# Performance work log

Hardware: AMD Instinct MI355X
Metric: run time of the kernel (lower is better)

## Reference

```python
import jax, jax.numpy as jnp
from jax import lax
import numpy as np

SIGMA = 5.0
ALPHA = 50.0
RADIUS = int(4.0 * SIGMA + 0.5)  # scipy gaussian_filter truncate=4.0 -> 20


def _gauss_kernel():
    t = jnp.arange(-RADIUS, RADIUS + 1, dtype=jnp.float32)
    phi = jnp.exp(-0.5 * (t / SIGMA) ** 2)
    return phi / phi.sum()


def _gaussian_blur(f):
    # f: [B, H, W]. scipy mode='reflect' (edge included) == jnp.pad mode='symmetric'.
    k = _gauss_kernel()
    K = 2 * RADIUS + 1
    fp = jnp.pad(f, ((0, 0), (RADIUS, RADIUS), (RADIUS, RADIUS)), mode='symmetric')[:, None]
    z = lax.conv_general_dilated(fp, k.reshape(1, 1, K, 1), (1, 1), 'VALID')
    z = lax.conv_general_dilated(z, k.reshape(1, 1, 1, K), (1, 1), 'VALID')
    return z[:, 0]


def _reflect(i, n):
    # scipy mode='reflect': (d c b a | a b c d | d c b a), period 2n on integer indices
    i = jnp.mod(i, 2 * n)
    return jnp.where(i >= n, 2 * n - 1 - i, i)


def _bilinear(img, yy, xx):
    # img: [H, W]; yy/xx: [H, W] float sample coords (rows, cols)
    H, W = img.shape
    y0 = jnp.floor(yy)
    x0 = jnp.floor(xx)
    wy = yy - y0
    wx = xx - x0
    y0i = y0.astype(jnp.int32)
    x0i = x0.astype(jnp.int32)
    y0r = _reflect(y0i, H)
    y1r = _reflect(y0i + 1, H)
    x0r = _reflect(x0i, W)
    x1r = _reflect(x0i + 1, W)
    v00 = img[y0r, x0r]
    v01 = img[y0r, x1r]
    v10 = img[y1r, x0r]
    v11 = img[y1r, x1r]
    return (v00 * (1 - wy) * (1 - wx) + v01 * (1 - wy) * wx
            + v10 * wy * (1 - wx) + v11 * wy * wx)


def setup_inputs() -> dict:
    key = jax.random.key(0)
    k1, k2, k3 = jax.random.split(key, 3)
    B, H, W = 64, 512, 512
    x = jax.random.normal(k1, (B, 1, H, W), dtype=jnp.float32)
    rand_dx = jax.random.uniform(k2, (B, H, W), dtype=jnp.float32)
    rand_dy = jax.random.uniform(k3, (B, H, W), dtype=jnp.float32)
    return {"x": x, "rand_dx": rand_dx, "rand_dy": rand_dy}


def reference(x, rand_dx, rand_dy):
    # x: [B, 1, H, W]
    B, C, H, W = x.shape
    dx = _gaussian_blur(rand_dx * 2.0 - 1.0) * ALPHA  # [B, H, W]
    dy = _gaussian_blur(rand_dy * 2.0 - 1.0) * ALPHA
    gx, gy = jnp.meshgrid(jnp.arange(W, dtype=x.dtype), jnp.arange(H, dtype=x.dtype))
    yy = gy[None] + dy  # row coords
    xx = gx[None] + dx  # col coords
    warped = jax.vmap(_bilinear)(x[:, 0], yy, xx)  # [B, H, W]
    return warped[:, None]
```

## Files before the change

### kernel.cpp

```cpp
#include <hip/hip_runtime.h>

#define RADIUS 20
#define KSIZE  41
#define ALPHA_F 50.0f
#define TY     8
#define WID    512
#define HEI    512
#define PW     (WID + 2 * RADIUS)
#define NR     (TY + 2 * RADIUS)
#define PF     8

__device__ constexpr float G[KSIZE] = {
    2.6770e-05f, 5.8390e-05f, 1.22380e-04f, 2.46460e-04f, 4.76840e-04f,
    8.86410e-04f, 1.583160e-03f, 2.716710e-03f, 4.479090e-03f, 7.095210e-03f,
    1.0798630e-02f, 1.5790680e-02f, 2.2185070e-02f, 2.9946720e-02f, 3.8838800e-02f,
    4.8396120e-02f, 5.7940680e-02f, 6.6647650e-02f, 7.3657040e-02f, 7.8211730e-02f,
    7.9791720e-02f,
    7.8211730e-02f, 7.3657040e-02f, 6.6647650e-02f, 5.7940680e-02f, 4.8396120e-02f,
    3.8838800e-02f, 2.9946720e-02f, 2.2185070e-02f, 1.5790680e-02f, 1.0798630e-02f,
    7.095210e-03f, 4.479090e-03f, 2.716710e-03f, 1.583160e-03f, 8.86410e-04f,
    4.76840e-04f, 2.46460e-04f, 1.22380e-04f, 5.8390e-05f, 2.6770e-05f
};

__device__ __forceinline__ int refl(int i, int n) {
    i = (i < 0) ? (-1 - i) : i;
    i = (i >= n) ? (2 * n - 1 - i) : i;
    return i;
}
__device__ __forceinline__ int clampi(int i, int n) {
    return (i < 0) ? 0 : ((i >= n) ? n - 1 : i);
}

__global__ __launch_bounds__(512) void elastic_kernel(
    const float* __restrict__ xin, const float* __restrict__ rdx,
    const float* __restrict__ rdy, float* __restrict__ outp, int B) {

    __shared__ float sdx[TY][PW];
    __shared__ float sdy[TY][PW];

    const int tid = threadIdx.x;

    int b, band;
    {
        const int L = blockIdx.x;
        if (B == 64) {
            const int xcd = L & 7;
            const int s   = L >> 3;
            b    = xcd * 8 + (s >> 6);
            band = s & 63;
        } else {
            b    = L / (HEI / TY);
            band = L % (HEI / TY);
        }
    }
    const int y0 = band * TY;
    const size_t base = (size_t)b * (HEI * WID);

    {
        const float* px = rdx + base + tid;
        const float* py = rdy + base + tid;

        float bx[PF], by[PF];
        #pragma unroll
        for (int k = 0; k < PF; ++k) {
            const int gy = refl(y0 - RADIUS + k, HEI);
            bx[k] = px[(size_t)gy * WID];
            by[k] = py[(size_t)gy * WID];
        }

        float ax[TY], ay[TY];
        #pragma unroll
        for (int o = 0; o < TY; ++o) { ax[o] = 0.f; ay[o] = 0.f; }

        #pragma unroll
        for (int r = 0; r < NR; ++r) {
            const float vx = bx[r & (PF - 1)];
            const float vy = by[r & (PF - 1)];
            if (r + PF < NR) {
                const int gy = refl(y0 - RADIUS + r + PF, HEI);
                bx[r & (PF - 1)] = px[(size_t)gy * WID];
                by[r & (PF - 1)] = py[(size_t)gy * WID];
            }
            #pragma unroll
            for (int o = 0; o < TY; ++o) {
                const int t = r - o;
                if (t >= 0 && t < KSIZE) {
                    ax[o] = fmaf(G[t], vx, ax[o]);
                    ay[o] = fmaf(G[t], vy, ay[o]);
                }
            }
        }

        #pragma unroll
        for (int o = 0; o < TY; ++o) {
            const float sx = 2.f * ax[o] - 1.f;
            const float sy = 2.f * ay[o] - 1.f;
            sdx[o][RADIUS + tid] = sx;
            sdy[o][RADIUS + tid] = sy;
            if (tid < RADIUS) {
                sdx[o][RADIUS - 1 - tid] = sx;
                sdy[o][RADIUS - 1 - tid] = sy;
            }
            if (tid >= WID - RADIUS) {
                sdx[o][RADIUS + 2 * WID - 1 - tid] = sx;
                sdy[o][RADIUS + 2 * WID - 1 - tid] = sy;
            }
        }
    }
    __syncthreads();

    const int c4 = tid & 127;
    const int rg = tid >> 7;
    const float* img = xin + base;

    #pragma unroll
    for (int i = 0; i < 2; ++i) {
        const int o  = rg + 4 * i;
        const int gy = y0 + o;

        float dxv[4] = {0.f, 0.f, 0.f, 0.f};
        float dyv[4] = {0.f, 0.f, 0.f, 0.f};

        {
            float w[44];
            const float4* rp = (const float4*)(&sdx[o][0]);
            #pragma unroll
            for (int q = 0; q < 11; ++q) {
                const float4 v = rp[c4 + q];
                w[4 * q + 0] = v.x; w[4 * q + 1] = v.y;
                w[4 * q + 2] = v.z; w[4 * q + 3] = v.w;
            }
            #pragma unroll
            for (int t = 0; t < KSIZE; ++t) {
                const float g = G[t];
                #pragma unroll
                for (int j = 0; j < 4; ++j) dxv[j] = fmaf(g, w[t + j], dxv[j]);
            }
        }
        {
            float w[44];
            const float4* rp = (const float4*)(&sdy[o][0]);
            #pragma unroll
            for (int q = 0; q < 11; ++q) {
                const float4 v = rp[c4 + q];
                w[4 * q + 0] = v.x; w[4 * q + 1] = v.y;
                w[4 * q + 2] = v.z; w[4 * q + 3] = v.w;
            }
            #pragma unroll
            for (int t = 0; t < KSIZE; ++t) {
                const float g = G[t];
                #pragma unroll
                for (int j = 0; j < 4; ++j) dyv[j] = fmaf(g, w[t + j], dyv[j]);
            }
        }

        float st[4];
        #pragma unroll
        for (int j = 0; j < 4; ++j) {
            const int col = 4 * c4 + j;
            float xx = (float)col + dxv[j] * ALPHA_F;
            float yy = (float)gy  + dyv[j] * ALPHA_F;
            xx = fminf(fmaxf(xx, -2048.f), 2048.f);
            yy = fminf(fmaxf(yy, -2048.f), 2048.f);
            const float x0f = floorf(xx), y0f = floorf(yy);
            const float wx = xx - x0f, wy = yy - y0f;
            const int x0 = (int)x0f, yb = (int)y0f;
            const int x0r = clampi(refl(x0, WID), WID);
            const int x1r = clampi(refl(x0 + 1, WID), WID);
            const int y0r = clampi(refl(yb, HEI), HEI);
            const int y1r = clampi(refl(yb + 1, HEI), HEI);

            const float v00 = img[(size_t)y0r * WID + x0r];
            const float v01 = img[(size_t)y0r * WID + x1r];
            const float v10 = img[(size_t)y1r * WID + x0r];
            const float v11 = img[(size_t)y1r * WID + x1r];

            st[j] = v00 * (1.f - wy) * (1.f - wx) + v01 * (1.f - wy) * wx
                  + v10 * wy * (1.f - wx) + v11 * wy * wx;
        }

        float4 pack;
        pack.x = st[0]; pack.y = st[1]; pack.z = st[2]; pack.w = st[3];
        *reinterpret_cast<float4*>(outp + base + (size_t)gy * WID + 4 * c4) = pack;
    }
}

extern "C" void kernel_launch(void* const* d_in, const int* in_sizes, int n_in,
                              void* d_out, int out_size, void* d_ws, size_t ws_size,
                              hipStream_t stream) {
    const float* x   = (const float*)d_in[0];
    const float* rdx = (const float*)d_in[1];
    const float* rdy = (const float*)d_in[2];
    float* out = (float*)d_out;

    const int B = in_sizes[1] / (HEI * WID);

    const int nblocks = B * (HEI / TY);
    elastic_kernel<<<nblocks, 512, 0, stream>>>(x, rdx, rdy, out, B);
    (void)d_ws; (void)ws_size; (void)n_in; (void)out_size;
}
```

Before: 288.1 us.

## Double band height and vectorize vertical blur with float4 per thread

```diff
diff --git a/kernel.cpp b/kernel.cpp
--- a/kernel.cpp
+++ b/kernel.cpp
@@ -3,11 +3,11 @@
 #define RADIUS 20
 #define KSIZE  41
 #define ALPHA_F 50.0f
-#define TY     8
+#define TY     16
 #define WID    512
 #define HEI    512
 #define PW     (WID + 2 * RADIUS)
-#define NR     (TY + 2 * RADIUS)
+#define NRH    48
 #define PF     8
 
 __device__ constexpr float G[KSIZE] = {
@@ -27,8 +27,43 @@
     i = (i >= n) ? (2 * n - 1 - i) : i;
     return i;
 }
-__device__ __forceinline__ int clampi(int i, int n) {
-    return (i < 0) ? 0 : ((i >= n) ? n - 1 : i);
+
+__device__ __forceinline__ int refl512(int i) {
+    i = (i < 0) ? (-1 - i) : i;
+    return (i >= 512) ? (1023 - i) : i;
+}
+
+template<bool INTERIOR>
+__device__ __forceinline__ void vblur8(const float* __restrict__ src, int ybase,
+                                       float acc[8][4]) {
+    float bx[PF][4];
+    #pragma unroll
+    for (int k = 0; k < PF; ++k) {
+        const int gy = INTERIOR ? (ybase + k) : refl(ybase + k, HEI);
+        const float4 v = *reinterpret_cast<const float4*>(src + (size_t)gy * WID);
+        bx[k][0] = v.x; bx[k][1] = v.y; bx[k][2] = v.z; bx[k][3] = v.w;
+    }
+    #pragma unroll
+    for (int r = 0; r < NRH; ++r) {
+        float v[4];
+        #pragma unroll
+        for (int j = 0; j < 4; ++j) v[j] = bx[r & (PF - 1)][j];
+        if (r + PF < NRH) {
+            const int gy = INTERIOR ? (ybase + r + PF) : refl(ybase + r + PF, HEI);
+            const float4 nv = *reinterpret_cast<const float4*>(src + (size_t)gy * WID);
+            bx[r & (PF - 1)][0] = nv.x; bx[r & (PF - 1)][1] = nv.y;
+            bx[r & (PF - 1)][2] = nv.z; bx[r & (PF - 1)][3] = nv.w;
+        }
+        #pragma unroll
+        for (int o = 0; o < 8; ++o) {
+            const int t = r - o;
+            if (t >= 0 && t < KSIZE) {
+                const float g = G[t];
+                #pragma unroll
+                for (int j = 0; j < 4; ++j) acc[o][j] = fmaf(g, v[j], acc[o][j]);
+            }
+        }
+    }
 }
 
 __global__ __launch_bounds__(512) void elastic_kernel(
@@ -46,8 +81,8 @@
         if (B == 64) {
             const int xcd = L & 7;
             const int s   = L >> 3;
-            b    = xcd * 8 + (s >> 6);
-            band = s & 63;
+            b    = xcd * 8 + (s >> 5);
+            band = s & 31;
         } else {
             b    = L / (HEI / TY);
             band = L % (HEI / TY);
@@ -57,53 +92,40 @@
     const size_t base = (size_t)b * (HEI * WID);
 
     {
-        const float* px = rdx + base + tid;
-        const float* py = rdy + base + tid;
-
-        float bx[PF], by[PF];
-        #pragma unroll
-        for (int k = 0; k < PF; ++k) {
-            const int gy = refl(y0 - RADIUS + k, HEI);
-            bx[k] = px[(size_t)gy * WID];
-            by[k] = py[(size_t)gy * WID];
-        }
-
-        float ax[TY], ay[TY];
-        #pragma unroll
-        for (int o = 0; o < TY; ++o) { ax[o] = 0.f; ay[o] = 0.f; }
-
-        #pragma unroll
-        for (int r = 0; r < NR; ++r) {
-            const float vx = bx[r & (PF - 1)];
-            const float vy = by[r & (PF - 1)];
-            if (r + PF < NR) {
-                const int gy = refl(y0 - RADIUS + r + PF, HEI);
-                bx[r & (PF - 1)] = px[(size_t)gy * WID];
-                by[r & (PF - 1)] = py[(size_t)gy * WID];
-            }
-            #pragma unroll
-            for (int o = 0; o < TY; ++o) {
-                const int t = r - o;
-                if (t >= 0 && t < KSIZE) {
-                    ax[o] = fmaf(G[t], vx, ax[o]);
-                    ay[o] = fmaf(G[t], vy, ay[o]);
-                }
-            }
-        }
-
-        #pragma unroll
-        for (int o = 0; o < TY; ++o) {
-            const float sx = 2.f * ax[o] - 1.f;
-            const float sy = 2.f * ay[o] - 1.f;
-            sdx[o][RADIUS + tid] = sx;
-            sdy[o][RADIUS + tid] = sy;
-            if (tid < RADIUS) {
-                sdx[o][RADIUS - 1 - tid] = sx;
-                sdy[o][RADIUS - 1 - tid] = sy;
-            }
-            if (tid >= WID - RADIUS) {
-                sdx[o][RADIUS + 2 * WID - 1 - tid] = sx;
-                sdy[o][RADIUS + 2 * WID - 1 - tid] = sy;
+        const int c4 = tid & 127;
+        const int f  = (tid >> 7) & 1;
+        const int h  = tid >> 8;
+        const int ybase = y0 + 8 * h - RADIUS;
+
+        const float* src = (f ? rdy : rdx) + base + 4 * c4;
+
+        float acc[8][4];
+        #pragma unroll
+        for (int o = 0; o < 8; ++o)
+            #pragma unroll
+            for (int j = 0; j < 4; ++j) acc[o][j] = 0.f;
+
+        if (ybase >= 0 && ybase + NRH <= HEI) vblur8<true >(src, ybase, acc);
+        else                                  vblur8<false>(src, ybase, acc);
+
+        float (*sd)[PW] = f ? sdy : sdx;
+
+        #pragma unroll
+        for (int o = 0; o < 8; ++o) {
+            const int row = 8 * h + o;
+            float sv[4];
+            #pragma unroll
+            for (int j = 0; j < 4; ++j) sv[j] = 2.f * acc[o][j] - 1.f;
+            float4 pack;
+            pack.x = sv[0]; pack.y = sv[1]; pack.z = sv[2]; pack.w = sv[3];
+            *reinterpret_cast<float4*>(&sd[row][RADIUS + 4 * c4]) = pack;
+            if (c4 < 5) {
+                #pragma unroll
+                for (int j = 0; j < 4; ++j) sd[row][RADIUS - 1 - (4 * c4 + j)] = sv[j];
+            }
+            if (c4 >= 123) {
+                #pragma unroll
+                for (int j = 0; j < 4; ++j) sd[row][RADIUS + 2 * WID - 1 - (4 * c4 + j)] = sv[j];
             }
         }
     }
@@ -114,7 +136,7 @@
     const float* img = xin + base;
 
     #pragma unroll
-    for (int i = 0; i < 2; ++i) {
+    for (int i = 0; i < 4; ++i) {
         const int o  = rg + 4 * i;
         const int gy = y0 + o;
 
@@ -160,23 +182,26 @@
             const int col = 4 * c4 + j;
             float xx = (float)col + dxv[j] * ALPHA_F;
             float yy = (float)gy  + dyv[j] * ALPHA_F;
-            xx = fminf(fmaxf(xx, -2048.f), 2048.f);
-            yy = fminf(fmaxf(yy, -2048.f), 2048.f);
+            xx = fminf(fmaxf(xx, -511.f), 1022.f);
+            yy = fminf(fmaxf(yy, -511.f), 1022.f);
             const float x0f = floorf(xx), y0f = floorf(yy);
             const float wx = xx - x0f, wy = yy - y0f;
             const int x0 = (int)x0f, yb = (int)y0f;
-            const int x0r = clampi(refl(x0, WID), WID);
-            const int x1r = clampi(refl(x0 + 1, WID), WID);
-            const int y0r = clampi(refl(yb, HEI), HEI);
-            const int y1r = clampi(refl(yb + 1, HEI), HEI);
-
-            const float v00 = img[(size_t)y0r * WID + x0r];
-            const float v01 = img[(size_t)y0r * WID + x1r];
-            const float v10 = img[(size_t)y1r * WID + x0r];
-            const float v11 = img[(size_t)y1r * WID + x1r];
-
-            st[j] = v00 * (1.f - wy) * (1.f - wx) + v01 * (1.f - wy) * wx
-                  + v10 * wy * (1.f - wx) + v11 * wy * wx;
+            const int x0r = refl512(x0);
+            const int x1r = refl512(x0 + 1);
+            const int y0r = refl512(yb);
+            const int y1r = refl512(yb + 1);
+
+            const float* r0 = img + ((size_t)y0r << 9);
+            const float* r1 = img + ((size_t)y1r << 9);
+            const float v00 = r0[x0r];
+            const float v01 = r0[x1r];
+            const float v10 = r1[x0r];
+            const float v11 = r1[x1r];
+
+            const float top = fmaf(wx, v01 - v00, v00);
+            const float bot = fmaf(wx, v11 - v10, v10);
+            st[j] = fmaf(wy, bot - top, top);
         }
 
         float4 pack;
```

Result: no change. 286.2 us (-0.7%).
